# Kernel tuning notes

Hardware: AMD Instinct MI355X
Metric: run time of the kernel (lower is better)

## Reference

```python
import jax, jax.numpy as jnp
import numpy as np

N_NODES = 50000
N_EDGES = 625000
HIDDEN = 128
NUM_GRAPHS = 128
EPS = 1e-5


def setup_inputs() -> dict:
    key = jax.random.key(0)
    ks = jax.random.split(key, 8)
    node = jax.random.normal(ks[0], (N_NODES, HIDDEN), dtype=jnp.float32)
    edge_index = jax.random.randint(ks[1], (2, N_EDGES), 0, N_NODES, dtype=jnp.int64)
    edge_attr = jax.random.uniform(ks[2], (N_EDGES,), dtype=jnp.float32)
    batch_ptr = jnp.sort(jax.random.randint(ks[3], (N_NODES,), 0, NUM_GRAPHS, dtype=jnp.int64))
    # GCNConv linear: weight [out,in], bias [out]
    W = jax.random.normal(ks[4], (HIDDEN, HIDDEN), dtype=jnp.float32) * (1.0 / np.sqrt(HIDDEN))
    b = jnp.zeros((HIDDEN,), dtype=jnp.float32)
    # GraphNorm params
    gn_weight = 1.0 + 0.02 * jax.random.normal(ks[5], (HIDDEN,), dtype=jnp.float32)
    gn_bias = 0.05 * jax.random.normal(ks[6], (HIDDEN,), dtype=jnp.float32)
    gn_mean_scale = 1.0 + 0.02 * jax.random.normal(ks[7], (HIDDEN,), dtype=jnp.float32)
    return {"node": node, "edge_index": edge_index, "edge_attr": edge_attr,
            "batch_ptr": batch_ptr, "W": W, "b": b,
            "gn_weight": gn_weight, "gn_bias": gn_bias, "gn_mean_scale": gn_mean_scale}


def _gcn_conv(x, src, dst, w, W, b):
    n = x.shape[0]
    # add self loops with weight 1
    loop = jnp.arange(n, dtype=src.dtype)
    src = jnp.concatenate([src, loop])
    dst = jnp.concatenate([dst, loop])
    w = jnp.concatenate([w, jnp.ones((n,), dtype=w.dtype)])
    # symmetric degree normalization (degrees at target nodes)
    deg = jax.ops.segment_sum(w, dst, num_segments=n)
    dinv = jnp.where(deg > 0, jax.lax.rsqrt(deg), 0.0)
    norm = dinv[src] * w * dinv[dst]  # [E+n]
    h = x @ W.T  # [n, d]
    msg = norm[:, None] * h[src]  # gather + scale
    out = jax.ops.segment_sum(msg, dst, num_segments=n)  # scatter-add
    return out + b


def _graph_norm(x, batch, weight, bias, mean_scale):
    cnt = jax.ops.segment_sum(jnp.ones((x.shape[0],), x.dtype), batch, num_segments=NUM_GRAPHS)
    cnt = jnp.maximum(cnt, 1.0)[:, None]
    mean = jax.ops.segment_sum(x, batch, num_segments=NUM_GRAPHS) / cnt
    centered = x - mean_scale * mean[batch]
    var = jax.ops.segment_sum(centered * centered, batch, num_segments=NUM_GRAPHS) / cnt
    inv_std = jax.lax.rsqrt(var + EPS)[batch]
    return weight * centered * inv_std + bias


def reference(node, edge_index, edge_attr, batch_ptr, W, b, gn_weight, gn_bias, gn_mean_scale):
    src, dst = edge_index[0], edge_index[1]
    h = _gcn_conv(node, src, dst, edge_attr, W, b)
    h = _graph_norm(h, batch_ptr, gn_weight, gn_bias, gn_mean_scale)
    return jax.nn.relu(h)
```

## Files before the change

### kernel.cpp

```cpp
#include <hip/hip_runtime.h>

#define N_NODES    50000
#define N_EDGES    625000
#define HIDDEN     128
#define NUM_GRAPHS 128
#define EPS_GN     1e-5f
#define FIXSCALE   1048576.0f
#define NGEMM_BLK  782
#define NHIST_BLK  306
#define NB_SCAN    196

typedef __bf16 bf16x8 __attribute__((ext_vector_type(8)));
typedef float  f32x4  __attribute__((ext_vector_type(4)));
typedef unsigned short u16x8 __attribute__((ext_vector_type(8)));
typedef unsigned long long u64;

__device__ inline unsigned short f2b(float f) {
    __bf16 b = (__bf16)f;
    return __builtin_bit_cast(unsigned short, b);
}
__device__ inline float b2f(unsigned short u) {
    unsigned int x = ((unsigned int)u) << 16;
    return __builtin_bit_cast(float, x);
}

#define HB_OFF     0
#define CNT64_OFF  3200000
#define DINV_OFF   3300000
#define WB_OFF     3352000
#define GSTART_OFF 3362000
#define ROWS_OFF   3363000
#define BSUM_OFF   3414000
#define EPACK_OFF  3414100
#define SLOT_OFF   4664100
#define TMP_OFF    5289104
#undef TMP_OFF
#define TMP_OFF    4664100

__global__ void prep(const float* __restrict__ W, unsigned short* __restrict__ wb,
                     uint4* __restrict__ cntz) {
    int i = blockIdx.x * 256 + threadIdx.x;
    if (i < 100000 / 4) cntz[i] = make_uint4(0u, 0u, 0u, 0u);
    if (i < HIDDEN * HIDDEN) wb[i] = f2b(W[i]);
}

__global__ __launch_bounds__(256) void gemm_hist(const float* __restrict__ x,
                                                 const unsigned short* __restrict__ wb,
                                                 unsigned short* __restrict__ hb,
                                                 const int* __restrict__ dst,
                                                 const float* __restrict__ w,
                                                 u64* __restrict__ cnt64,
                                                 unsigned int* __restrict__ slot) {
    if (blockIdx.x >= NGEMM_BLK) {
        int base = (blockIdx.x - NGEMM_BLK) * 256 + threadIdx.x;
        if (base * 8 >= N_EDGES) return;
        int4   dA = ((const int4*)dst)[base * 2];
        int4   dB = ((const int4*)dst)[base * 2 + 1];
        float4 wA = ((const float4*)w)[base * 2];
        float4 wB = ((const float4*)w)[base * 2 + 1];
        uint4 sA, sB;
        {
            unsigned int fx = (unsigned int)(wA.x * FIXSCALE + 0.5f);
            sA.x = (unsigned int)(atomicAdd(&cnt64[dA.x], (1ULL << 32) | (u64)fx) >> 32);
            fx = (unsigned int)(wA.y * FIXSCALE + 0.5f);
            sA.y = (unsigned int)(atomicAdd(&cnt64[dA.y], (1ULL << 32) | (u64)fx) >> 32);
            fx = (unsigned int)(wA.z * FIXSCALE + 0.5f);
            sA.z = (unsigned int)(atomicAdd(&cnt64[dA.z], (1ULL << 32) | (u64)fx) >> 32);
            fx = (unsigned int)(wA.w * FIXSCALE + 0.5f);
            sA.w = (unsigned int)(atomicAdd(&cnt64[dA.w], (1ULL << 32) | (u64)fx) >> 32);
            fx = (unsigned int)(wB.x * FIXSCALE + 0.5f);
            sB.x = (unsigned int)(atomicAdd(&cnt64[dB.x], (1ULL << 32) | (u64)fx) >> 32);
            fx = (unsigned int)(wB.y * FIXSCALE + 0.5f);
            sB.y = (unsigned int)(atomicAdd(&cnt64[dB.y], (1ULL << 32) | (u64)fx) >> 32);
            fx = (unsigned int)(wB.z * FIXSCALE + 0.5f);
            sB.z = (unsigned int)(atomicAdd(&cnt64[dB.z], (1ULL << 32) | (u64)fx) >> 32);
            fx = (unsigned int)(wB.w * FIXSCALE + 0.5f);
            sB.w = (unsigned int)(atomicAdd(&cnt64[dB.w], (1ULL << 32) | (u64)fx) >> 32);
        }
        ((uint4*)slot)[base * 2]     = sA;
        ((uint4*)slot)[base * 2 + 1] = sB;
        return;
    }
    const int wave = threadIdx.x >> 6;
    const int lane = threadIdx.x & 63;
    const int row0 = blockIdx.x * 64 + wave * 16;
    const int r  = lane & 15;
    const int ko = (lane >> 4) * 8;
    f32x4 acc[8];
#pragma unroll
    for (int t = 0; t < 8; ++t) { acc[t][0] = 0.f; acc[t][1] = 0.f; acc[t][2] = 0.f; acc[t][3] = 0.f; }
    int arow = row0 + r;
    if (arow >= N_NODES) arow = N_NODES - 1;
    const size_t abase = (size_t)arow * HIDDEN + ko;
#pragma unroll
    for (int kt = 0; kt < HIDDEN; kt += 32) {
        float4 a0 = *(const float4*)(x + abase + kt);
        float4 a1 = *(const float4*)(x + abase + kt + 4);
        bf16x8 a;
        a[0] = (__bf16)a0.x; a[1] = (__bf16)a0.y; a[2] = (__bf16)a0.z; a[3] = (__bf16)a0.w;
        a[4] = (__bf16)a1.x; a[5] = (__bf16)a1.y; a[6] = (__bf16)a1.z; a[7] = (__bf16)a1.w;
#pragma unroll
        for (int t = 0; t < 8; ++t) {
            bf16x8 b = *(const bf16x8*)(wb + (size_t)(t * 16 + r) * HIDDEN + kt + ko);
            acc[t] = __builtin_amdgcn_mfma_f32_16x16x32_bf16(a, b, acc[t], 0, 0, 0);
        }
    }
    const int orow = row0 + (lane >> 4) * 4;
#pragma unroll
    for (int t = 0; t < 8; ++t) {
#pragma unroll
        for (int j = 0; j < 4; ++j) {
            int rr = orow + j;
            if (rr < N_NODES) hb[(size_t)rr * HIDDEN + t * 16 + r] = f2b(acc[t][j]);
        }
    }
}

__global__ void scan_partial(const u64* __restrict__ cnt64, int* __restrict__ bsum,
                             float* __restrict__ dinv,
                             const int* __restrict__ batch, int* __restrict__ gstart) {
    __shared__ int red[256];
    int i = blockIdx.x * 256 + threadIdx.x;
    int c = 0;
    if (i < N_NODES) {
        u64 v = cnt64[i];
        c = (int)(v >> 32);
        dinv[i] = rsqrtf(1.0f + (float)(unsigned int)v * (1.0f / FIXSCALE));
        int b0 = batch[i];
        int prev = (i == 0) ? -1 : batch[i - 1];
        for (int g = prev + 1; g <= b0; ++g) gstart[g] = i;
        if (i == N_NODES - 1) {
            for (int g = b0 + 1; g <= NUM_GRAPHS; ++g) gstart[g] = N_NODES;
        }
    }
    red[threadIdx.x] = c;
    __syncthreads();
    for (int off = 128; off > 0; off >>= 1) {
        if (threadIdx.x < off) red[threadIdx.x] += red[threadIdx.x + off];
        __syncthreads();
    }
    if (threadIdx.x == 0) bsum[blockIdx.x] = red[0];
}

__global__ void scan_emit(const u64* __restrict__ cnt64, const int* __restrict__ bsum,
                          int* __restrict__ rowstart) {
    __shared__ int sb[256];
    __shared__ int s[256];
    int t = threadIdx.x;
    sb[t] = (t < NB_SCAN) ? bsum[t] : 0;
    __syncthreads();
    for (int off = 1; off < 256; off <<= 1) {
        int v = (t >= off) ? sb[t - off] : 0;
        __syncthreads();
        sb[t] += v;
        __syncthreads();
    }
    int boff = (blockIdx.x == 0) ? 0 : sb[blockIdx.x - 1];
    int i = blockIdx.x * 256 + t;
    int v0 = (i < N_NODES) ? (int)(cnt64[i] >> 32) : 0;
    s[t] = v0;
    __syncthreads();
    for (int off = 1; off < 256; off <<= 1) {
        int v = (t >= off) ? s[t - off] : 0;
        __syncthreads();
        s[t] += v;
        __syncthreads();
    }
    if (i < N_NODES) rowstart[i] = boff + s[t] - v0;
    if (i == N_NODES) rowstart[N_NODES] = N_EDGES;
}

__global__ void csr_fill(const int* __restrict__ src, const int* __restrict__ dst,
                         const float* __restrict__ w, const float* __restrict__ dinv,
                         const int* __restrict__ rowstart, const unsigned int* __restrict__ slot,
                         u64* __restrict__ epack) {
    int base = blockIdx.x * blockDim.x + threadIdx.x;
    if (base * 4 >= N_EDGES) return;
    int4   s4 = ((const int4*)src)[base];
    int4   d4 = ((const int4*)dst)[base];
    float4 w4 = ((const float4*)w)[base];
    uint4  r4 = ((const uint4*)slot)[base];
    float nm0 = dinv[s4.x] * w4.x * dinv[d4.x];
    float nm1 = dinv[s4.y] * w4.y * dinv[d4.y];
    float nm2 = dinv[s4.z] * w4.z * dinv[d4.z];
    float nm3 = dinv[s4.w] * w4.w * dinv[d4.w];
    epack[rowstart[d4.x] + (int)r4.x] = (u64)(unsigned int)s4.x | ((u64)__float_as_uint(nm0) << 32);
    epack[rowstart[d4.y] + (int)r4.y] = (u64)(unsigned int)s4.y | ((u64)__float_as_uint(nm1) << 32);
    epack[rowstart[d4.z] + (int)r4.z] = (u64)(unsigned int)s4.z | ((u64)__float_as_uint(nm2) << 32);
    epack[rowstart[d4.w] + (int)r4.w] = (u64)(unsigned int)s4.w | ((u64)__float_as_uint(nm3) << 32);
}

__global__ __launch_bounds__(256) void gather_fused(const unsigned short* __restrict__ hb,
                                                    const int* __restrict__ rowstart,
                                                    const u64* __restrict__ epack,
                                                    const float* __restrict__ dinv,
                                                    const float* __restrict__ b,
                                                    unsigned short* __restrict__ tmp) {
    const int t = threadIdx.x;
    const int n = blockIdx.x * 16 + (t >> 4);
    if (n >= N_NODES) return;
    const int c8 = (t & 15) * 8;
    const int s0 = rowstart[n];
    const int e0 = rowstart[n + 1];
    const float di = dinv[n];
    const float sl = di * di;
    float acc[8];
    {
        u16x8 hv = *(const u16x8*)(hb + (size_t)n * HIDDEN + c8);
#pragma unroll
        for (int j = 0; j < 8; ++j) acc[j] = sl * b2f(hv[j]);
    }
    int p = s0;
    for (; p + 4 <= e0; p += 4) {
        u64 e1 = epack[p];
        u64 e2 = epack[p + 1];
        u64 e3 = epack[p + 2];
        u64 e4 = epack[p + 3];
        int   x1 = (int)(unsigned int)e1;
        int   x2 = (int)(unsigned int)e2;
        int   x3 = (int)(unsigned int)e3;
        int   x4 = (int)(unsigned int)e4;
        float n1 = __uint_as_float((unsigned int)(e1 >> 32));
        float n2 = __uint_as_float((unsigned int)(e2 >> 32));
        float n3 = __uint_as_float((unsigned int)(e3 >> 32));
        float n4 = __uint_as_float((unsigned int)(e4 >> 32));
        u16x8 v1 = *(const u16x8*)(hb + (size_t)x1 * HIDDEN + c8);
        u16x8 v2 = *(const u16x8*)(hb + (size_t)x2 * HIDDEN + c8);
        u16x8 v3 = *(const u16x8*)(hb + (size_t)x3 * HIDDEN + c8);
        u16x8 v4 = *(const u16x8*)(hb + (size_t)x4 * HIDDEN + c8);
#pragma unroll
        for (int j = 0; j < 8; ++j) acc[j] = fmaf(n1, b2f(v1[j]), acc[j]);
#pragma unroll
        for (int j = 0; j < 8; ++j) acc[j] = fmaf(n2, b2f(v2[j]), acc[j]);
#pragma unroll
        for (int j = 0; j < 8; ++j) acc[j] = fmaf(n3, b2f(v3[j]), acc[j]);
#pragma unroll
        for (int j = 0; j < 8; ++j) acc[j] = fmaf(n4, b2f(v4[j]), acc[j]);
    }
    for (; p < e0; ++p) {
        u64 e1 = epack[p];
        int   x1 = (int)(unsigned int)e1;
        float n1 = __uint_as_float((unsigned int)(e1 >> 32));
        u16x8 v1 = *(const u16x8*)(hb + (size_t)x1 * HIDDEN + c8);
#pragma unroll
        for (int j = 0; j < 8; ++j) acc[j] = fmaf(n1, b2f(v1[j]), acc[j]);
    }
    float4 b0 = *(const float4*)(b + c8);
    float4 b1 = *(const float4*)(b + c8 + 4);
    u16x8 o;
    o[0] = f2b(acc[0] + b0.x); o[1] = f2b(acc[1] + b0.y);
    o[2] = f2b(acc[2] + b0.z); o[3] = f2b(acc[3] + b0.w);
    o[4] = f2b(acc[4] + b1.x); o[5] = f2b(acc[5] + b1.y);
    o[6] = f2b(acc[6] + b1.z); o[7] = f2b(acc[7] + b1.w);
    *(u16x8*)(tmp + (size_t)n * HIDDEN + c8) = o;
}

__global__ __launch_bounds__(256) void stats_apply(const unsigned short* __restrict__ tmp,
                                                   const int* __restrict__ gstart,
                                                   const float* __restrict__ ms,
                                                   const float* __restrict__ gw,
                                                   const float* __restrict__ gb,
                                                   float* __restrict__ out) {
    const int g = blockIdx.x >> 2;
    const int q = blockIdx.x & 3;
    const int l = threadIdx.x & 31;
    const int c = q * 32 + l;
    const int r = threadIdx.x >> 5;
    const int s = gstart[g];
    const int e = gstart[g + 1];
    float sum = 0.f, sq = 0.f;
    for (int n = s + r; n < e; n += 8) {
        float v = b2f(tmp[(size_t)n * HIDDEN + c]);
        sum += v;
        sq = fmaf(v, v, sq);
    }
    __shared__ float ssum[8][32], ssq[8][32];
    __shared__ float sA[32], sS[32];
    ssum[r][l] = sum;
    ssq[r][l]  = sq;
    __syncthreads();
    if (r == 0) {
#pragma unroll
        for (int i = 1; i < 8; ++i) { sum += ssum[i][l]; sq += ssq[i][l]; }
        float cnt  = (float)max(e - s, 1);
        float mean = sum / cnt;
        float m2   = sq / cnt;
        float msv  = ms[c];
        float var  = fmaxf(m2 - mean * mean * msv * (2.f - msv), 0.f);
        float a    = gw[c] * rsqrtf(var + EPS_GN);
        sA[l] = a;
        sS[l] = gb[c] - a * msv * mean;
    }
    __syncthreads();
    float a  = sA[l];
    float sh = sS[l];
    for (int n = s + r; n < e; n += 8) {
        float v = b2f(tmp[(size_t)n * HIDDEN + c]);
        out[(size_t)n * HIDDEN + c] = fmaxf(fmaf(a, v, sh), 0.f);
    }
}

extern "C" void kernel_launch(void* const* d_in, const int* in_sizes, int n_in,
                              void* d_out, int out_size, void* d_ws, size_t ws_size,
                              hipStream_t stream) {
    const float* node  = (const float*)d_in[0];
    const int*   ei    = (const int*)d_in[1];
    const float* eattr = (const float*)d_in[2];
    const int*   batch = (const int*)d_in[3];
    const float* W     = (const float*)d_in[4];
    const float* b     = (const float*)d_in[5];
    const float* gnw   = (const float*)d_in[6];
    const float* gnb   = (const float*)d_in[7];
    const float* gnms  = (const float*)d_in[8];
    float* out = (float*)d_out;
    float* ws  = (float*)d_ws;

    const int* src = ei;
    const int* dst = ei + N_EDGES;

    unsigned short* hb = (unsigned short*)(ws + HB_OFF);
    u64*   cnt64   = (u64*)(ws + CNT64_OFF);
    float* dinv    = ws + DINV_OFF;
    unsigned short* wb = (unsigned short*)(ws + WB_OFF);
    int*   gstart  = (int*)(ws + GSTART_OFF);
    int*   rowstart= (int*)(ws + ROWS_OFF);
    int*   bsum    = (int*)(ws + BSUM_OFF);
    u64*   epack   = (u64*)(ws + EPACK_OFF);
    unsigned int* slot = (unsigned int*)(ws + SLOT_OFF);
    unsigned short* tmp = (unsigned short*)(ws + TMP_OFF);

    prep<<<98, 256, 0, stream>>>(W, wb, (uint4*)cnt64);
    gemm_hist<<<NGEMM_BLK + NHIST_BLK, 256, 0, stream>>>(node, wb, hb, dst, eattr, cnt64, slot);
    scan_partial<<<NB_SCAN, 256, 0, stream>>>(cnt64, bsum, dinv, batch, gstart);
    scan_emit<<<NB_SCAN, 256, 0, stream>>>(cnt64, bsum, rowstart);
    csr_fill<<<(N_EDGES / 4 + 255) / 256, 256, 0, stream>>>(src, dst, eattr, dinv, rowstart, slot, epack);
    gather_fused<<<(N_NODES + 15) / 16, 256, 0, stream>>>(hb, rowstart, epack, dinv, b, tmp);
    stats_apply<<<NUM_GRAPHS * 4, 256, 0, stream>>>(tmp, gstart, gnms, gnw, gnb, out);

    (void)in_sizes; (void)n_in; (void)out_size; (void)ws_size;
}
```

Before: 124.5 us.

## Pack degree histogram into 32-bit atomics and fuse scan kernels via grid barrier

Switches the per-node count and weight-sum accumulator from 64-bit to 32-bit atomics, with the count in the top 8 bits and a 16.16 fixed-point weight sum in the low 24 bits. This halves atomic traffic and the zeroing work. It also merges scan_partial and scan_emit into one kernel that uses a software grid barrier on a done counter, removing one launch and a reread of the counts. The packing risks overflow if any node has more than 255 in-edges or a weight sum of 256 or more, and it coarsens weight precision. The spin barrier relies on all 196 blocks being co-resident.

```diff
diff --git a/kernel.cpp b/kernel.cpp
--- a/kernel.cpp
+++ b/kernel.cpp
@@ -5,7 +5,7 @@
 #define HIDDEN     128
 #define NUM_GRAPHS 128
 #define EPS_GN     1e-5f
-#define FIXSCALE   1048576.0f
+#define FIXSCALE32 65536.0f
 #define NGEMM_BLK  782
 #define NHIST_BLK  306
 #define NB_SCAN    196
@@ -25,22 +25,21 @@
 }
 
 #define HB_OFF     0
-#define CNT64_OFF  3200000
-#define DINV_OFF   3300000
-#define WB_OFF     3352000
-#define GSTART_OFF 3362000
-#define ROWS_OFF   3363000
-#define BSUM_OFF   3414000
-#define EPACK_OFF  3414100
-#define SLOT_OFF   4664100
-#define TMP_OFF    5289104
-#undef TMP_OFF
-#define TMP_OFF    4664100
+#define CNT_OFF    3200000
+#define BSUM_OFF   3250000
+#define DONE_OFF   3250256
+#define DINV_OFF   3250260
+#define WB_OFF     3300260
+#define GSTART_OFF 3308452
+#define ROWS_OFF   3308581
+#define EPACK_OFF  3358582
+#define SLOT_OFF   4608582
+#define TMP_OFF    4608584
 
 __global__ void prep(const float* __restrict__ W, unsigned short* __restrict__ wb,
-                     uint4* __restrict__ cntz) {
+                     uint4* __restrict__ z) {
     int i = blockIdx.x * 256 + threadIdx.x;
-    if (i < 100000 / 4) cntz[i] = make_uint4(0u, 0u, 0u, 0u);
+    if (i < 12565) z[i] = make_uint4(0u, 0u, 0u, 0u);
     if (i < HIDDEN * HIDDEN) wb[i] = f2b(W[i]);
 }
 
@@ -49,7 +48,7 @@
                                                  unsigned short* __restrict__ hb,
                                                  const int* __restrict__ dst,
                                                  const float* __restrict__ w,
-                                                 u64* __restrict__ cnt64,
+                                                 unsigned int* __restrict__ cnt32,
                                                  unsigned int* __restrict__ slot) {
     if (blockIdx.x >= NGEMM_BLK) {
         int base = (blockIdx.x - NGEMM_BLK) * 256 + threadIdx.x;
@@ -59,24 +58,23 @@
         float4 wA = ((const float4*)w)[base * 2];
         float4 wB = ((const float4*)w)[base * 2 + 1];
         uint4 sA, sB;
-        {
-            unsigned int fx = (unsigned int)(wA.x * FIXSCALE + 0.5f);
-            sA.x = (unsigned int)(atomicAdd(&cnt64[dA.x], (1ULL << 32) | (u64)fx) >> 32);
-            fx = (unsigned int)(wA.y * FIXSCALE + 0.5f);
-            sA.y = (unsigned int)(atomicAdd(&cnt64[dA.y], (1ULL << 32) | (u64)fx) >> 32);
-            fx = (unsigned int)(wA.z * FIXSCALE + 0.5f);
-            sA.z = (unsigned int)(atomicAdd(&cnt64[dA.z], (1ULL << 32) | (u64)fx) >> 32);
-            fx = (unsigned int)(wA.w * FIXSCALE + 0.5f);
-            sA.w = (unsigned int)(atomicAdd(&cnt64[dA.w], (1ULL << 32) | (u64)fx) >> 32);
-            fx = (unsigned int)(wB.x * FIXSCALE + 0.5f);
-            sB.x = (unsigned int)(atomicAdd(&cnt64[dB.x], (1ULL << 32) | (u64)fx) >> 32);
-            fx = (unsigned int)(wB.y * FIXSCALE + 0.5f);
-            sB.y = (unsigned int)(atomicAdd(&cnt64[dB.y], (1ULL << 32) | (u64)fx) >> 32);
-            fx = (unsigned int)(wB.z * FIXSCALE + 0.5f);
-            sB.z = (unsigned int)(atomicAdd(&cnt64[dB.z], (1ULL << 32) | (u64)fx) >> 32);
-            fx = (unsigned int)(wB.w * FIXSCALE + 0.5f);
-            sB.w = (unsigned int)(atomicAdd(&cnt64[dB.w], (1ULL << 32) | (u64)fx) >> 32);
-        }
+        unsigned int fx;
+        fx = (unsigned int)(wA.x * FIXSCALE32 + 0.5f);
+        sA.x = atomicAdd(&cnt32[dA.x], (1u << 24) | fx) >> 24;
+        fx = (unsigned int)(wA.y * FIXSCALE32 + 0.5f);
+        sA.y = atomicAdd(&cnt32[dA.y], (1u << 24) | fx) >> 24;
+        fx = (unsigned int)(wA.z * FIXSCALE32 + 0.5f);
+        sA.z = atomicAdd(&cnt32[dA.z], (1u << 24) | fx) >> 24;
+        fx = (unsigned int)(wA.w * FIXSCALE32 + 0.5f);
+        sA.w = atomicAdd(&cnt32[dA.w], (1u << 24) | fx) >> 24;
+        fx = (unsigned int)(wB.x * FIXSCALE32 + 0.5f);
+        sB.x = atomicAdd(&cnt32[dB.x], (1u << 24) | fx) >> 24;
+        fx = (unsigned int)(wB.y * FIXSCALE32 + 0.5f);
+        sB.y = atomicAdd(&cnt32[dB.y], (1u << 24) | fx) >> 24;
+        fx = (unsigned int)(wB.z * FIXSCALE32 + 0.5f);
+        sB.z = atomicAdd(&cnt32[dB.z], (1u << 24) | fx) >> 24;
+        fx = (unsigned int)(wB.w * FIXSCALE32 + 0.5f);
+        sB.w = atomicAdd(&cnt32[dB.w], (1u << 24) | fx) >> 24;
         ((uint4*)slot)[base * 2]     = sA;
         ((uint4*)slot)[base * 2 + 1] = sB;
         return;
@@ -116,16 +114,23 @@
     }
 }
 
-__global__ void scan_partial(const u64* __restrict__ cnt64, int* __restrict__ bsum,
-                             float* __restrict__ dinv,
-                             const int* __restrict__ batch, int* __restrict__ gstart) {
+__global__ __launch_bounds__(256) void scan_fused(const unsigned int* __restrict__ cnt32,
+                                                  unsigned int* __restrict__ bsum,
+                                                  unsigned int* __restrict__ done,
+                                                  float* __restrict__ dinv,
+                                                  const int* __restrict__ batch,
+                                                  int* __restrict__ gstart,
+                                                  int* __restrict__ rowstart) {
     __shared__ int red[256];
-    int i = blockIdx.x * 256 + threadIdx.x;
+    __shared__ int sb[256];
+    const int t = threadIdx.x;
+    const int b = blockIdx.x;
+    const int i = b * 256 + t;
     int c = 0;
     if (i < N_NODES) {
-        u64 v = cnt64[i];
-        c = (int)(v >> 32);
-        dinv[i] = rsqrtf(1.0f + (float)(unsigned int)v * (1.0f / FIXSCALE));
+        unsigned int v = cnt32[i];
+        c = (int)(v >> 24);
+        dinv[i] = rsqrtf(1.0f + (float)(v & 0xFFFFFFu) * (1.0f / FIXSCALE32));
         int b0 = batch[i];
         int prev = (i == 0) ? -1 : batch[i - 1];
         for (int g = prev + 1; g <= b0; ++g) gstart[g] = i;
@@ -133,21 +138,20 @@
             for (int g = b0 + 1; g <= NUM_GRAPHS; ++g) gstart[g] = N_NODES;
         }
     }
-    red[threadIdx.x] = c;
+    red[t] = c;
     __syncthreads();
     for (int off = 128; off > 0; off >>= 1) {
-        if (threadIdx.x < off) red[threadIdx.x] += red[threadIdx.x + off];
-        __syncthreads();
-    }
-    if (threadIdx.x == 0) bsum[blockIdx.x] = red[0];
-}
-
-__global__ void scan_emit(const u64* __restrict__ cnt64, const int* __restrict__ bsum,
-                          int* __restrict__ rowstart) {
-    __shared__ int sb[256];
-    __shared__ int s[256];
-    int t = threadIdx.x;
-    sb[t] = (t < NB_SCAN) ? bsum[t] : 0;
+        if (t < off) red[t] += red[t + off];
+        __syncthreads();
+    }
+    if (t == 0) {
+        atomicExch(&bsum[b], (unsigned int)red[0]);
+        __threadfence();
+        atomicAdd(done, 1u);
+        while (atomicAdd(done, 0u) < (unsigned int)NB_SCAN) { }
+    }
+    __syncthreads();
+    sb[t] = (t < NB_SCAN) ? (int)atomicAdd(&bsum[t], 0u) : 0;
     __syncthreads();
     for (int off = 1; off < 256; off <<= 1) {
         int v = (t >= off) ? sb[t - off] : 0;
@@ -155,10 +159,9 @@
         sb[t] += v;
         __syncthreads();
     }
-    int boff = (blockIdx.x == 0) ? 0 : sb[blockIdx.x - 1];
-    int i = blockIdx.x * 256 + t;
-    int v0 = (i < N_NODES) ? (int)(cnt64[i] >> 32) : 0;
-    s[t] = v0;
+    int boff = (b == 0) ? 0 : sb[b - 1];
+    __shared__ int s[256];
+    s[t] = c;
     __syncthreads();
     for (int off = 1; off < 256; off <<= 1) {
         int v = (t >= off) ? s[t - off] : 0;
@@ -166,7 +169,7 @@
         s[t] += v;
         __syncthreads();
     }
-    if (i < N_NODES) rowstart[i] = boff + s[t] - v0;
+    if (i < N_NODES) rowstart[i] = boff + s[t] - c;
     if (i == N_NODES) rowstart[N_NODES] = N_EDGES;
 }
 
@@ -319,20 +322,20 @@
     const int* dst = ei + N_EDGES;
 
     unsigned short* hb = (unsigned short*)(ws + HB_OFF);
-    u64*   cnt64   = (u64*)(ws + CNT64_OFF);
+    unsigned int* cnt32 = (unsigned int*)(ws + CNT_OFF);
+    unsigned int* bsum  = (unsigned int*)(ws + BSUM_OFF);
+    unsigned int* done  = (unsigned int*)(ws + DONE_OFF);
     float* dinv    = ws + DINV_OFF;
     unsigned short* wb = (unsigned short*)(ws + WB_OFF);
     int*   gstart  = (int*)(ws + GSTART_OFF);
     int*   rowstart= (int*)(ws + ROWS_OFF);
-    int*   bsum    = (int*)(ws + BSUM_OFF);
     u64*   epack   = (u64*)(ws + EPACK_OFF);
     unsigned int* slot = (unsigned int*)(ws + SLOT_OFF);
     unsigned short* tmp = (unsigned short*)(ws + TMP_OFF);
 
-    prep<<<98, 256, 0, stream>>>(W, wb, (uint4*)cnt64);
-    gemm_hist<<<NGEMM_BLK + NHIST_BLK, 256, 0, stream>>>(node, wb, hb, dst, eattr, cnt64, slot);
-    scan_partial<<<NB_SCAN, 256, 0, stream>>>(cnt64, bsum, dinv, batch, gstart);
-    scan_emit<<<NB_SCAN, 256, 0, stream>>>(cnt64, bsum, rowstart);
+    prep<<<98, 256, 0, stream>>>(W, wb, (uint4*)cnt32);
+    gemm_hist<<<NGEMM_BLK + NHIST_BLK, 256, 0, stream>>>(node, wb, hb, dst, eattr, cnt32, slot);
+    scan_fused<<<NB_SCAN, 256, 0, stream>>>(cnt32, bsum, done, dinv, batch, gstart, rowstart);
     csr_fill<<<(N_EDGES / 4 + 255) / 256, 256, 0, stream>>>(src, dst, eattr, dinv, rowstart, slot, epack);
     gather_fused<<<(N_NODES + 15) / 16, 256, 0, stream>>>(hb, rowstart, epack, dinv, b, tmp);
     stats_apply<<<NUM_GRAPHS * 4, 256, 0, stream>>>(tmp, gstart, gnms, gnw, gnb, out);
```

Result: slower. 127.2 us (+2.2%).
